# Kernel optimization log

Hardware: AMD Instinct MI355X
Metric: run time of the kernel (lower is better)

The kernel has to match this reference:

```python
import jax, jax.numpy as jnp
import numpy as np
import math

N_HEADS = 16


def setup_inputs() -> dict:
    key = jax.random.key(0)
    ks = jax.random.split(key, 6)
    B, S, D = 2, 2048, 2048
    hd = D // N_HEADS  # 128
    scale = 0.02
    x = jax.random.normal(ks[0], (B, S, D), dtype=jnp.float32)
    wq = jax.random.normal(ks[1], (D, D), dtype=jnp.float32) * scale
    wk = jax.random.normal(ks[2], (D, D), dtype=jnp.float32) * scale
    wv = jax.random.normal(ks[3], (D, D), dtype=jnp.float32) * scale
    wo = jax.random.normal(ks[4], (D, D), dtype=jnp.float32) * scale
    # Rotary frequencies: theta = 10000^(-2i/hd), angle[t, i] = t * theta_i
    inv_freq = 1.0 / (10000.0 ** (jnp.arange(0, hd, 2, dtype=jnp.float32) / hd))  # [hd//2]
    angles = jnp.arange(S, dtype=jnp.float32)[:, None] * inv_freq[None, :]  # [S, hd//2]
    freqs_cos = jnp.cos(angles)
    freqs_sin = jnp.sin(angles)
    # Causal additive mask [1,1,S,S]
    causal = jnp.tril(jnp.ones((S, S), dtype=bool))
    mask = jnp.where(causal, 0.0, -1e9).astype(jnp.float32)[None, None]
    return {"x": x, "wq": wq, "wk": wk, "wv": wv, "wo": wo,
            "freqs_cos": freqs_cos, "freqs_sin": freqs_sin, "mask": mask}


def _apply_rope(t, cos, sin):
    # t: [B,S,H,hd]; cos/sin: [S, hd//2]. Complex mult on (even, odd) pairs.
    B, S, H, hd = t.shape
    tr = t.reshape(B, S, H, hd // 2, 2)
    t0, t1 = tr[..., 0], tr[..., 1]
    c = cos[None, :, None, :]
    s = sin[None, :, None, :]
    o0 = t0 * c - t1 * s
    o1 = t0 * s + t1 * c
    return jnp.stack([o0, o1], axis=-1).reshape(B, S, H, hd)


def reference(x, wq, wk, wv, wo, freqs_cos, freqs_sin, mask):
    B, S, D = x.shape
    H = N_HEADS
    hd = D // H
    # Projections (torch Linear: y = x @ W^T)
    q = jnp.einsum('bsd,ed->bse', x, wq).reshape(B, S, H, hd)
    k = jnp.einsum('bsd,ed->bse', x, wk).reshape(B, S, H, hd)
    v = jnp.einsum('bsd,ed->bse', x, wv).reshape(B, S, H, hd)
    q = _apply_rope(q, freqs_cos, freqs_sin)
    k = _apply_rope(k, freqs_cos, freqs_sin)
    # Attention: scores [B,H,S,S]
    scores = jnp.einsum('bshd,bthd->bhst', q, k) / math.sqrt(hd)
    scores = scores + mask[:, :, :S, :S]
    attn = jax.nn.softmax(scores.astype(jnp.float32), axis=-1).astype(q.dtype)
    out = jnp.einsum('bhst,bthd->bshd', attn, v).reshape(B, S, D)
    return jnp.einsum('bsd,ed->bse', out, wo)
```

## Files before the change

kernel.cpp:

```cpp
#include <hip/hip_runtime.h>

typedef unsigned short u16;
typedef __attribute__((ext_vector_type(8))) short short8;
typedef __attribute__((ext_vector_type(4))) short short4s;
typedef __attribute__((ext_vector_type(4))) float f32x4;

__device__ __forceinline__ u16 f2b(float f) {
  union { float f; unsigned u; } c; c.f = f;
  unsigned u = c.u;
  unsigned r = (u + 0x7FFFu + ((u >> 16) & 1u)) >> 16;
  return (u16)r;
}
__device__ __forceinline__ float b2f(u16 h) {
  union { unsigned u; float f; } c; c.u = ((unsigned)h) << 16;
  return c.f;
}

__device__ __forceinline__ void gload16(const u16* g, u16* l) {
  __builtin_amdgcn_global_load_lds((const __attribute__((address_space(1))) void*)g,
                                   (__attribute__((address_space(3))) void*)l, 16, 0, 0);
}

__device__ __forceinline__ short4s tr16(const u16* p) {
  short4s d;
  asm volatile("ds_read_b64_tr_b16 %0, %1"
               : "=v"(d)
               : "v"((const __attribute__((address_space(3))) u16*)p));
  return d;
}

#define MFMA(a, b, c) __builtin_amdgcn_mfma_f32_16x16x32_bf16(a, b, c, 0, 0, 0)

__global__ __launch_bounds__(256) void cast_f32_bf16(const float4* __restrict__ in,
                                                     u16* __restrict__ out, int n4) {
  int i = blockIdx.x * 256 + threadIdx.x;
  if (i >= n4) return;
  float4 v = in[i];
  ushort4 r;
  r.x = f2b(v.x); r.y = f2b(v.y); r.z = f2b(v.z); r.w = f2b(v.w);
  *(ushort4*)(out + (size_t)i * 4) = r;
}

__global__ __launch_bounds__(256) void rope_k(u16* __restrict__ qkv,
                                              const float* __restrict__ fc,
                                              const float* __restrict__ fs) {
  int idx = blockIdx.x * 256 + threadIdx.x;
  int m = idx >> 8;
  int c = idx & 255;
  int s = m & 2047;
  int i0 = (c * 4) & 63;
  u16* p = qkv + (size_t)m * 6144 + 2048 + c * 8;
  short8 v = *(short8*)p;
  float4 cs = *(const float4*)(fc + (size_t)s * 64 + i0);
  float4 sn = *(const float4*)(fs + (size_t)s * 64 + i0);
  float cc[4] = {cs.x, cs.y, cs.z, cs.w};
  float ss[4] = {sn.x, sn.y, sn.z, sn.w};
#pragma unroll
  for (int t = 0; t < 4; ++t) {
    float x0 = b2f((u16)v[2 * t]);
    float x1 = b2f((u16)v[2 * t + 1]);
    float o0 = x0 * cc[t] - x1 * ss[t];
    float o1 = x0 * ss[t] + x1 * cc[t];
    v[2 * t]     = (short)f2b(o0);
    v[2 * t + 1] = (short)f2b(o1);
  }
  *(short8*)p = v;
}

template <int F32OUT>
__global__ __launch_bounds__(512, 4) void gemm_nt_2ph(const u16* __restrict__ Ag,
                                                      const u16* __restrict__ Bg,
                                                      void* __restrict__ Cp,
                                                      int M, int N, int K) {
  __shared__ __align__(16) u16 lds[24576];
  const int tid = threadIdx.x;
  const int l = tid & 63, w = tid >> 6;
  const int wm = w >> 2, wn = w & 3;
  const int ln = l & 15, lk = l >> 4;
  const int nbn = N >> 8;
  const int nwg = (M >> 7) * nbn;
  const int wg = ((blockIdx.x & 7) * (nwg >> 3)) + (blockIdx.x >> 3);
  const int row0 = (wg / nbn) << 7;
  const int col0 = (wg % nbn) << 8;
  const int T = K >> 5;

  const int r0s = tid >> 2;
  const int j0s = ((tid & 3) ^ (r0s & 3)) << 3;

#define STAGE_A(t)                                                                    \
  gload16(Ag + (size_t)(row0 + r0s) * K + (t) * 32 + j0s,                             \
          lds + ((t) & 1) * 4096 + tid * 8);
#define STAGE_B(t, h)                                                                 \
  gload16(Bg + (size_t)(col0 + (h) * 128 + r0s) * K + (t) * 32 + j0s,                 \
          lds + 8192 + ((t) & 1) * 8192 + (h) * 4096 + tid * 8);

  f32x4 acc[4][4];
#pragma unroll
  for (int m = 0; m < 4; ++m)
#pragma unroll
    for (int n = 0; n < 4; ++n) acc[m][n] = (f32x4){0.f, 0.f, 0.f, 0.f};

  const int cx = ((lk ^ (ln & 3)) << 3);

  STAGE_A(0); STAGE_B(0, 0); STAGE_B(0, 1);
  STAGE_A(1); STAGE_B(1, 0); STAGE_B(1, 1);
  asm volatile("s_waitcnt vmcnt(3)" ::: "memory");
  __builtin_amdgcn_s_barrier();

  for (int t = 0; t < T; ++t) {
    const u16* aB = lds + (t & 1) * 4096;
    const u16* bB = lds + 8192 + (t & 1) * 8192 + (wn >> 1) * 4096;
    short8 bf[4];
    short8 af[2];
#pragma unroll
    for (int q = 0; q < 2; ++q) {
      if (q == 0) {
#pragma unroll
        for (int n = 0; n < 4; ++n)
          bf[n] = *(const short8*)&bB[((wn & 1) * 64 + n * 16 + ln) * 32 + cx];
      }
#pragma unroll
      for (int m2 = 0; m2 < 2; ++m2)
        af[m2] = *(const short8*)&aB[(wm * 64 + (q * 2 + m2) * 16 + ln) * 32 + cx];
      if (q == 0) {
        if (t >= 1 && t + 1 < T) STAGE_A(t + 1);
      } else {
        if (t + 2 < T) {
          STAGE_B(t + 2, 0);
          STAGE_B(t + 2, 1);
          asm volatile("s_waitcnt vmcnt(2)" ::: "memory");
        } else if (t + 1 < T) {
          asm volatile("s_waitcnt vmcnt(0)" ::: "memory");
        }
      }
      __builtin_amdgcn_sched_barrier(0);
      __builtin_amdgcn_s_barrier();
      __builtin_amdgcn_sched_barrier(0);
      __builtin_amdgcn_s_setprio(1);
#pragma unroll
      for (int m2 = 0; m2 < 2; ++m2)
#pragma unroll
        for (int n = 0; n < 4; ++n)
          acc[q * 2 + m2][n] = MFMA(af[m2], bf[n], acc[q * 2 + m2][n]);
      __builtin_amdgcn_s_setprio(0);
      __builtin_amdgcn_sched_barrier(0);
      __builtin_amdgcn_s_barrier();
      __builtin_amdgcn_sched_barrier(0);
    }
  }

#pragma unroll
  for (int m = 0; m < 4; ++m) {
    int r0 = row0 + wm * 64 + m * 16 + lk * 4;
#pragma unroll
    for (int n = 0; n < 4; ++n) {
      int cc = col0 + wn * 64 + n * 16 + ln;
#pragma unroll
      for (int j = 0; j < 4; ++j) {
        float v = acc[m][n][j];
        if (F32OUT) ((float*)Cp)[(size_t)(r0 + j) * N + cc] = v;
        else        ((u16*)Cp)[(size_t)(r0 + j) * N + cc]   = f2b(v);
      }
    }
  }
#undef STAGE_A
#undef STAGE_B
}

__global__ __launch_bounds__(256) void attn_fwd(const u16* __restrict__ qkv,
                                                const float* __restrict__ fc,
                                                const float* __restrict__ fs,
                                                u16* __restrict__ out) {
  __shared__ __align__(16) u16 sK[2][64 * 128];
  __shared__ __align__(16) u16 sV[2][64 * 128];
  __shared__ __align__(16) u16 sP[4][16 * 72];
  const int tid = threadIdx.x, l = tid & 63, w = tid >> 6;
  const int ln = l & 15, lk = l >> 4;

  const int bid = blockIdx.x;
  const int l0 = ((bid & 7) << 6) + (bid >> 3);
  const int bh = l0 >> 4, pr = l0 & 15;
  const int b = bh >> 4, h = bh & 15;

  const u16* Kp = qkv + (size_t)b * 2048 * 6144 + 2048 + h * 128;
  const u16* Vp = Kp + 2048;
  const float scale = 0.08838834764831845f;

  for (int pass = 0; pass < 2; ++pass) {
    const int qt = pass ? (31 - pr) : pr;
    const int m0 = b * 2048 + qt * 64;
    const u16* Qp = qkv + (size_t)m0 * 6144 + h * 128;
    const int srow = qt * 64 + w * 16 + ln;

    short8 qf[4];
#pragma unroll
    for (int kc = 0; kc < 4; ++kc) {
      short8 raw = *(const short8*)(Qp + (size_t)(w * 16 + ln) * 6144 + kc * 32 + lk * 8);
      float4 c4 = *(const float4*)(fc + (size_t)srow * 64 + kc * 16 + lk * 4);
      float4 s4 = *(const float4*)(fs + (size_t)srow * 64 + kc * 16 + lk * 4);
      float cc[4] = {c4.x * scale, c4.y * scale, c4.z * scale, c4.w * scale};
      float ss[4] = {s4.x * scale, s4.y * scale, s4.z * scale, s4.w * scale};
#pragma unroll
      for (int t = 0; t < 4; ++t) {
        float x0 = b2f((u16)raw[2 * t]);
        float x1 = b2f((u16)raw[2 * t + 1]);
        qf[kc][2 * t]     = (short)f2b(x0 * cc[t] - x1 * ss[t]);
        qf[kc][2 * t + 1] = (short)f2b(x0 * ss[t] + x1 * cc[t]);
      }
    }

    f32x4 o[8];
#pragma unroll
    for (int d = 0; d < 8; ++d) o[d] = (f32x4){0.f, 0.f, 0.f, 0.f};
    float mrow[4] = {-1e9f, -1e9f, -1e9f, -1e9f};
    float lsum[4] = {0.f, 0.f, 0.f, 0.f};

    const int ntl = qt + 1;

    {
#pragma unroll
      for (int q = 0; q < 4; ++q) {
        int e = q * 256 + tid;
        int r = e >> 4, p = e & 15;
        gload16(Kp + (size_t)r * 6144 + ((p ^ (r & 7)) << 3), &sK[0][e * 8]);
        int j = ((e >> 6) << 2) + ((e & 7) >> 1);
        int d = (((e >> 3) & 7) << 4) + ((e & 1) << 3);
        gload16(Vp + (size_t)j * 6144 + d, &sV[0][e * 8]);
      }
    }
    __syncthreads();

    int cur = 0;
    for (int jt = 0; jt < ntl; ++jt) {
      if (jt + 1 < ntl) {
        const u16* Kt = Kp + (size_t)(jt + 1) * 64 * 6144;
        const u16* Vt = Vp + (size_t)(jt + 1) * 64 * 6144;
        int nb = cur ^ 1;
#pragma unroll
        for (int q = 0; q < 4; ++q) {
          int e = q * 256 + tid;
          int r = e >> 4, p = e & 15;
          gload16(Kt + (size_t)r * 6144 + ((p ^ (r & 7)) << 3), &sK[nb][e * 8]);
          int j = ((e >> 6) << 2) + ((e & 7) >> 1);
          int d = (((e >> 3) & 7) << 4) + ((e & 1) << 3);
          gload16(Vt + (size_t)j * 6144 + d, &sV[nb][e * 8]);
        }
      }

      f32x4 sf[4];
      __builtin_amdgcn_s_setprio(1);
#pragma unroll
      for (int nc = 0; nc < 4; ++nc) {
        f32x4 s = (f32x4){0.f, 0.f, 0.f, 0.f};
#pragma unroll
        for (int kc = 0; kc < 4; ++kc) {
          int r = nc * 16 + ln;
          short8 kb = *(const short8*)&sK[cur][r * 128 + (((kc << 2) + lk) ^ (r & 7)) * 8];
          s = MFMA(qf[kc], kb, s);
        }
        sf[nc] = s;
      }
      __builtin_amdgcn_s_setprio(0);

      if (jt == qt) {
        int ig = w * 16 + lk * 4;
#pragma unroll
        for (int nc = 0; nc < 4; ++nc) {
          int jg = nc * 16 + ln;
#pragma unroll
          for (int j = 0; j < 4; ++j)
            sf[nc][j] = (jg > ig + j) ? -1e9f : sf[nc][j];
        }
      }

      float tm[4];
#pragma unroll
      for (int j = 0; j < 4; ++j)
        tm[j] = fmaxf(fmaxf(sf[0][j], sf[1][j]), fmaxf(sf[2][j], sf[3][j]));
      int ok = (tm[0] <= mrow[0] + 8.f) & (tm[1] <= mrow[1] + 8.f) &
               (tm[2] <= mrow[2] + 8.f) & (tm[3] <= mrow[3] + 8.f);
      if (!__all(ok)) {
#pragma unroll
        for (int off = 1; off < 16; off <<= 1)
#pragma unroll
          for (int j = 0; j < 4; ++j) tm[j] = fmaxf(tm[j], __shfl_xor(tm[j], off, 16));
        float al[4];
#pragma unroll
        for (int j = 0; j < 4; ++j) {
          float nm = fmaxf(mrow[j], tm[j]);
          al[j] = __expf(mrow[j] - nm);
          mrow[j] = nm;
        }
#pragma unroll
        for (int d = 0; d < 8; ++d)
#pragma unroll
          for (int j = 0; j < 4; ++j) o[d][j] *= al[j];
#pragma unroll
        for (int j = 0; j < 4; ++j) lsum[j] *= al[j];
      }

#pragma unroll
      for (int nc = 0; nc < 4; ++nc)
#pragma unroll
        for (int j = 0; j < 4; ++j) {
          float p = __expf(sf[nc][j] - mrow[j]);
          u16 pb = f2b(p);
          sP[w][(lk * 4 + j) * 72 + nc * 16 + ln] = pb;
          lsum[j] += b2f(pb);
        }

      short8 pa0 = *(const short8*)&sP[w][ln * 72 + lk * 8];
      short8 pa1 = *(const short8*)&sP[w][ln * 72 + 32 + lk * 8];
      asm volatile("s_waitcnt lgkmcnt(0)" ::: "memory");
      __builtin_amdgcn_sched_barrier(0);

      short4s tb[4][4];
#define TRISSUE(dblk, slot)                                                  \
      {                                                                      \
        const u16* vb = &sV[cur][(lk * 2) * 512 + (dblk) * 64 + ln * 4];     \
        tb[slot][0] = tr16(vb);                                              \
        tb[slot][1] = tr16(vb + 512);                                        \
        tb[slot][2] = tr16(vb + 4096);                                       \
        tb[slot][3] = tr16(vb + 4096 + 512);                                 \
      }
      TRISSUE(0, 0);
      TRISSUE(1, 1);
      __builtin_amdgcn_s_setprio(1);
#pragma unroll
      for (int d = 0; d < 8; ++d) {
        if (d < 6) TRISSUE(d + 2, (d + 2) & 3);
        if (d < 6)       asm volatile("s_waitcnt lgkmcnt(8)" ::: "memory");
        else if (d == 6) asm volatile("s_waitcnt lgkmcnt(4)" ::: "memory");
        else             asm volatile("s_waitcnt lgkmcnt(0)" ::: "memory");
        __builtin_amdgcn_sched_barrier(0);
        short8 vb0 = {tb[d & 3][0][0], tb[d & 3][0][1], tb[d & 3][0][2], tb[d & 3][0][3],
                      tb[d & 3][1][0], tb[d & 3][1][1], tb[d & 3][1][2], tb[d & 3][1][3]};
        short8 vb1 = {tb[d & 3][2][0], tb[d & 3][2][1], tb[d & 3][2][2], tb[d & 3][2][3],
                      tb[d & 3][3][0], tb[d & 3][3][1], tb[d & 3][3][2], tb[d & 3][3][3]};
        o[d] = MFMA(pa0, vb0, o[d]);
        o[d] = MFMA(pa1, vb1, o[d]);
      }
      __builtin_amdgcn_s_setprio(0);
#undef TRISSUE

      __syncthreads();
      cur ^= 1;
    }

#pragma unroll
    for (int off = 1; off < 16; off <<= 1)
#pragma unroll
      for (int j = 0; j < 4; ++j) lsum[j] += __shfl_xor(lsum[j], off, 16);
    float inv[4];
#pragma unroll
    for (int j = 0; j < 4; ++j) inv[j] = 1.f / lsum[j];
#pragma unroll
    for (int d = 0; d < 8; ++d)
#pragma unroll
      for (int j = 0; j < 4; ++j)
        out[(size_t)(m0 + w * 16 + lk * 4 + j) * 2048 + h * 128 + d * 16 + ln] =
            f2b(o[d][j] * inv[j]);
  }
}

extern "C" void kernel_launch(void* const* d_in, const int* in_sizes, int n_in,
                              void* d_out, int out_size, void* d_ws, size_t ws_size,
                              hipStream_t stream) {
  const float* x  = (const float*)d_in[0];
  const float* wq = (const float*)d_in[1];
  const float* wk = (const float*)d_in[2];
  const float* wv = (const float*)d_in[3];
  const float* wo = (const float*)d_in[4];
  const float* fc = (const float*)d_in[5];
  const float* fs = (const float*)d_in[6];

  char* ws = (char*)d_ws;
  u16* xb   = (u16*)(ws);
  u16* wqkv = (u16*)(ws + 16777216);
  u16* wob  = (u16*)(ws + 41943040);
  u16* qkv  = (u16*)(ws + 50331648);
  u16* aout = (u16*)(ws + 100663296);

  cast_f32_bf16<<<8192, 256, 0, stream>>>((const float4*)x, xb, 2097152);
  cast_f32_bf16<<<4096, 256, 0, stream>>>((const float4*)wq, wqkv, 1048576);
  cast_f32_bf16<<<4096, 256, 0, stream>>>((const float4*)wk, wqkv + 4194304, 1048576);
  cast_f32_bf16<<<4096, 256, 0, stream>>>((const float4*)wv, wqkv + 8388608, 1048576);
  cast_f32_bf16<<<4096, 256, 0, stream>>>((const float4*)wo, wob, 1048576);

  gemm_nt_2ph<0><<<768, 512, 0, stream>>>(xb, wqkv, qkv, 4096, 6144, 2048);
  rope_k<<<4096, 256, 0, stream>>>(qkv, fc, fs);
  attn_fwd<<<512, 256, 0, stream>>>(qkv, fc, fs, aout);
  gemm_nt_2ph<1><<<256, 512, 0, stream>>>(aout, wob, d_out, 4096, 2048, 2048);
}
```

Baseline: 279.6 us.

## Load GEMM A operand directly to registers and merge cast kernels

The GEMM no longer stages the A tile through LDS. Each wave loads its A fragments straight from global memory into registers, double-buffered one K-step ahead, while B stays double-buffered in LDS. This cuts LDS use and removes one LDS round trip and one barrier phase per K-step. The cost is uncoalesced per-lane global reads of A, which are 16-byte row strips, and each A row is reread by the four waves that share it. The five f32-to-bf16 cast launches are also merged into one kernel to reduce launch overhead.

```diff
diff --git a/kernel.cpp b/kernel.cpp
--- a/kernel.cpp
+++ b/kernel.cpp
@@ -31,14 +31,25 @@
 
 #define MFMA(a, b, c) __builtin_amdgcn_mfma_f32_16x16x32_bf16(a, b, c, 0, 0, 0)
 
-__global__ __launch_bounds__(256) void cast_f32_bf16(const float4* __restrict__ in,
-                                                     u16* __restrict__ out, int n4) {
+__global__ __launch_bounds__(256) void cast_all(const float* __restrict__ x,
+                                                const float* __restrict__ wq,
+                                                const float* __restrict__ wk,
+                                                const float* __restrict__ wv,
+                                                const float* __restrict__ wo,
+                                                u16* __restrict__ xb,
+                                                u16* __restrict__ wqkv,
+                                                u16* __restrict__ wob) {
   int i = blockIdx.x * 256 + threadIdx.x;
-  if (i >= n4) return;
-  float4 v = in[i];
+  const float4* s; u16* d; int off;
+  if (i < 2097152)      { s = (const float4*)x;  d = xb;            off = i; }
+  else if (i < 3145728) { s = (const float4*)wq; d = wqkv;          off = i - 2097152; }
+  else if (i < 4194304) { s = (const float4*)wk; d = wqkv + 4194304; off = i - 3145728; }
+  else if (i < 5242880) { s = (const float4*)wv; d = wqkv + 8388608; off = i - 4194304; }
+  else                  { s = (const float4*)wo; d = wob;           off = i - 5242880; }
+  float4 v = s[off];
   ushort4 r;
   r.x = f2b(v.x); r.y = f2b(v.y); r.z = f2b(v.z); r.w = f2b(v.w);
-  *(ushort4*)(out + (size_t)i * 4) = r;
+  *(ushort4*)(d + (size_t)off * 4) = r;
 }
 
 __global__ __launch_bounds__(256) void rope_k(u16* __restrict__ qkv,
@@ -68,11 +79,11 @@
 }
 
 template <int F32OUT>
-__global__ __launch_bounds__(512, 4) void gemm_nt_2ph(const u16* __restrict__ Ag,
-                                                      const u16* __restrict__ Bg,
-                                                      void* __restrict__ Cp,
-                                                      int M, int N, int K) {
-  __shared__ __align__(16) u16 lds[24576];
+__global__ __launch_bounds__(512, 4) void gemm_ad(const u16* __restrict__ Ag,
+                                                  const u16* __restrict__ Bg,
+                                                  void* __restrict__ Cp,
+                                                  int M, int N, int K) {
+  __shared__ __align__(16) u16 lds[16384];
   const int tid = threadIdx.x;
   const int l = tid & 63, w = tid >> 6;
   const int wm = w >> 2, wn = w & 3;
@@ -87,12 +98,9 @@
   const int r0s = tid >> 2;
   const int j0s = ((tid & 3) ^ (r0s & 3)) << 3;
 
-#define STAGE_A(t)                                                                    \
-  gload16(Ag + (size_t)(row0 + r0s) * K + (t) * 32 + j0s,                             \
-          lds + ((t) & 1) * 4096 + tid * 8);
 #define STAGE_B(t, h)                                                                 \
   gload16(Bg + (size_t)(col0 + (h) * 128 + r0s) * K + (t) * 32 + j0s,                 \
-          lds + 8192 + ((t) & 1) * 8192 + (h) * 4096 + tid * 8);
+          lds + ((t) & 1) * 8192 + (h) * 4096 + tid * 8);
 
   f32x4 acc[4][4];
 #pragma unroll
@@ -101,52 +109,57 @@
     for (int n = 0; n < 4; ++n) acc[m][n] = (f32x4){0.f, 0.f, 0.f, 0.f};
 
   const int cx = ((lk ^ (ln & 3)) << 3);
-
-  STAGE_A(0); STAGE_B(0, 0); STAGE_B(0, 1);
-  STAGE_A(1); STAGE_B(1, 0); STAGE_B(1, 1);
-  asm volatile("s_waitcnt vmcnt(3)" ::: "memory");
+  const u16* abase = Ag + (size_t)(row0 + wm * 64 + ln) * K + lk * 8;
+
+  short8 af0[4], af1[4];
+
+  STAGE_B(0, 0); STAGE_B(0, 1);
+#pragma unroll
+  for (int m = 0; m < 4; ++m) af0[m] = *(const short8*)(abase + (size_t)m * 16 * K);
+  STAGE_B(1, 0); STAGE_B(1, 1);
+  asm volatile("s_waitcnt vmcnt(2)" ::: "memory");
+  __builtin_amdgcn_sched_barrier(0);
   __builtin_amdgcn_s_barrier();
-
-  for (int t = 0; t < T; ++t) {
-    const u16* aB = lds + (t & 1) * 4096;
-    const u16* bB = lds + 8192 + (t & 1) * 8192 + (wn >> 1) * 4096;
-    short8 bf[4];
-    short8 af[2];
-#pragma unroll
-    for (int q = 0; q < 2; ++q) {
-      if (q == 0) {
-#pragma unroll
-        for (int n = 0; n < 4; ++n)
-          bf[n] = *(const short8*)&bB[((wn & 1) * 64 + n * 16 + ln) * 32 + cx];
-      }
-#pragma unroll
-      for (int m2 = 0; m2 < 2; ++m2)
-        af[m2] = *(const short8*)&aB[(wm * 64 + (q * 2 + m2) * 16 + ln) * 32 + cx];
-      if (q == 0) {
-        if (t >= 1 && t + 1 < T) STAGE_A(t + 1);
-      } else {
-        if (t + 2 < T) {
-          STAGE_B(t + 2, 0);
-          STAGE_B(t + 2, 1);
-          asm volatile("s_waitcnt vmcnt(2)" ::: "memory");
-        } else if (t + 1 < T) {
-          asm volatile("s_waitcnt vmcnt(0)" ::: "memory");
-        }
-      }
-      __builtin_amdgcn_sched_barrier(0);
-      __builtin_amdgcn_s_barrier();
-      __builtin_amdgcn_sched_barrier(0);
-      __builtin_amdgcn_s_setprio(1);
-#pragma unroll
-      for (int m2 = 0; m2 < 2; ++m2)
-#pragma unroll
-        for (int n = 0; n < 4; ++n)
-          acc[q * 2 + m2][n] = MFMA(af[m2], bf[n], acc[q * 2 + m2][n]);
-      __builtin_amdgcn_s_setprio(0);
-      __builtin_amdgcn_sched_barrier(0);
-      __builtin_amdgcn_s_barrier();
-      __builtin_amdgcn_sched_barrier(0);
-    }
+  __builtin_amdgcn_sched_barrier(0);
+
+#define TILE(t, AFC, AFN)                                                             \
+  {                                                                                   \
+    const u16* bB = lds + ((t) & 1) * 8192 + (wn >> 1) * 4096;                        \
+    short8 bf[4];                                                                     \
+    _Pragma("unroll")                                                                 \
+    for (int n = 0; n < 4; ++n)                                                       \
+      bf[n] = *(const short8*)&bB[((wn & 1) * 64 + n * 16 + ln) * 32 + cx];           \
+    if ((t) + 1 < T) {                                                                \
+      _Pragma("unroll")                                                               \
+      for (int m = 0; m < 4; ++m)                                                     \
+        AFN[m] = *(const short8*)(abase + (size_t)m * 16 * K + ((t) + 1) * 32);       \
+    }                                                                                 \
+    __builtin_amdgcn_sched_barrier(0);                                                \
+    __builtin_amdgcn_s_setprio(1);                                                    \
+    _Pragma("unroll")                                                                 \
+    for (int m = 0; m < 4; ++m)                                                       \
+      _Pragma("unroll")                                                               \
+      for (int n = 0; n < 4; ++n)                                                     \
+        acc[m][n] = MFMA(AFC[m], bf[n], acc[m][n]);                                   \
+    __builtin_amdgcn_s_setprio(0);                                                    \
+    __builtin_amdgcn_sched_barrier(0);                                                \
+    __builtin_amdgcn_s_barrier();                                                     \
+    __builtin_amdgcn_sched_barrier(0);                                                \
+    if ((t) + 2 < T) {                                                                \
+      STAGE_B((t) + 2, 0);                                                            \
+      STAGE_B((t) + 2, 1);                                                            \
+      asm volatile("s_waitcnt vmcnt(2)" ::: "memory");                                \
+    } else {                                                                          \
+      asm volatile("s_waitcnt vmcnt(0)" ::: "memory");                                \
+    }                                                                                 \
+    __builtin_amdgcn_sched_barrier(0);                                                \
+    __builtin_amdgcn_s_barrier();                                                     \
+    __builtin_amdgcn_sched_barrier(0);                                                \
+  }
+
+  for (int t = 0; t < T; t += 2) {
+    TILE(t, af0, af1);
+    TILE(t + 1, af1, af0);
   }
 
 #pragma unroll
@@ -163,7 +176,7 @@
       }
     }
   }
-#undef STAGE_A
+#undef TILE
 #undef STAGE_B
 }
 
@@ -381,14 +394,9 @@
   u16* qkv  = (u16*)(ws + 50331648);
   u16* aout = (u16*)(ws + 100663296);
 
-  cast_f32_bf16<<<8192, 256, 0, stream>>>((const float4*)x, xb, 2097152);
-  cast_f32_bf16<<<4096, 256, 0, stream>>>((const float4*)wq, wqkv, 1048576);
-  cast_f32_bf16<<<4096, 256, 0, stream>>>((const float4*)wk, wqkv + 4194304, 1048576);
-  cast_f32_bf16<<<4096, 256, 0, stream>>>((const float4*)wv, wqkv + 8388608, 1048576);
-  cast_f32_bf16<<<4096, 256, 0, stream>>>((const float4*)wo, wob, 1048576);
-
-  gemm_nt_2ph<0><<<768, 512, 0, stream>>>(xb, wqkv, qkv, 4096, 6144, 2048);
+  cast_all<<<24576, 256, 0, stream>>>(x, wq, wk, wv, wo, xb, wqkv, wob);
+  gemm_ad<0><<<768, 512, 0, stream>>>(xb, wqkv, qkv, 4096, 6144, 2048);
   rope_k<<<4096, 256, 0, stream>>>(qkv, fc, fs);
   attn_fwd<<<512, 256, 0, stream>>>(qkv, fc, fs, aout);
-  gemm_nt_2ph<1><<<256, 512, 0, stream>>>(aout, wob, d_out, 4096, 2048, 2048);
-}
+  gemm_ad<1><<<256, 512, 0, stream>>>(aout, wob, d_out, 4096, 2048, 2048);
+}
```

Result: slower. 513.6 us (+83.7%).
